# Optimization experiments

Measured on AMD Instinct MI355X. Metric: run time of the kernel, lower is better.

## Reference

```python
import jax, jax.numpy as jnp
import numpy as np

B, T, D, NH = 4, 2048, 1024, 16
HD = D // NH


def setup_inputs() -> dict:
    key = jax.random.key(0)
    ks = jax.random.split(key, 6)
    scale = 0.02
    x = jax.random.normal(ks[0], (B, T, D), dtype=jnp.float32)
    Wr = jax.random.normal(ks[1], (D, D), dtype=jnp.float32) * scale
    Wk = jax.random.normal(ks[2], (D, D), dtype=jnp.float32) * scale
    Wv = jax.random.normal(ks[3], (D, D), dtype=jnp.float32) * scale
    Ww = jax.random.normal(ks[4], (D, D), dtype=jnp.float32) * scale
    Wo = jax.random.normal(ks[5], (D, D), dtype=jnp.float32) * scale
    return {"x": x, "Wr": Wr, "Wk": Wk, "Wv": Wv, "Ww": Ww, "Wo": Wo}


def _rwkv7_forward(x, Wr, Wk, Wv, Ww, Wo):
    b, t, d = x.shape
    nh, hd = NH, d // NH
    # projections (F.linear: x @ W.T), no bias
    r = jax.nn.sigmoid(x @ Wr.T).reshape(b, t, nh, hd)
    k = (x @ Wk.T).reshape(b, t, nh, hd)
    v = (x @ Wv.T).reshape(b, t, nh, hd)
    w = (jax.nn.sigmoid(x @ Ww.T) * 0.99).reshape(b, t, nh, hd)

    def step(state, inp):
        # state: [B, nh, hd_v, hd_k]
        w_t, k_t, v_t, r_t = inp  # each [B, nh, hd]
        state = state * w_t[..., :, None] + v_t[..., :, None] * k_t[..., None, :]
        out_t = r_t * state.sum(-1)  # [B, nh, hd]
        return state, out_t

    seq = (jnp.moveaxis(w, 1, 0), jnp.moveaxis(k, 1, 0),
           jnp.moveaxis(v, 1, 0), jnp.moveaxis(r, 1, 0))  # time-major
    state0 = jnp.zeros((b, nh, hd, hd), dtype=x.dtype)
    _, outs = jax.lax.scan(step, state0, seq)  # [T, B, nh, hd]
    out = jnp.moveaxis(outs, 0, 1).reshape(b, t, d)

    # RMSNorm with eps=None -> torch uses dtype eps
    eps = jnp.asarray(jnp.finfo(out.dtype).eps, out.dtype)
    out = out * jax.lax.rsqrt(jnp.mean(out * out, axis=-1, keepdims=True) + eps)
    return out @ Wo.T


def reference(x, Wr, Wk, Wv, Ww, Wo):
    return _rwkv7_forward(x, Wr, Wk, Wv, Ww, Wo)
```

## Files before the change

### kernel.cpp

```cpp
#include <hip/hip_runtime.h>
#include <hip/hip_bf16.h>
#include <stdint.h>


#define BB 4
#define TT 2048
#define DD 1024
#define NHH 16
#define HDD 64
#define CC 64
#define LL 32
#define NCH 4096

using bf16 = __hip_bfloat16;
typedef __attribute__((ext_vector_type(8))) short bfrag8;
typedef __attribute__((ext_vector_type(4))) float f32x4;

__device__ __forceinline__ void async_ld16(const bf16* g, bf16* l) {
  __builtin_amdgcn_global_load_lds(
      (const __attribute__((address_space(1))) uint32_t*)g,
      (__attribute__((address_space(3))) uint32_t*)l, 16, 0, 0);
}

__device__ __forceinline__ float sigm(float x) {
  return __builtin_amdgcn_rcpf(1.0f + __expf(-x));
}
__device__ __forceinline__ float bf2f(bf16 h) {
  unsigned short u = *reinterpret_cast<unsigned short*>(&h);
  return __uint_as_float((unsigned)u << 16);
}
__device__ __forceinline__ unsigned short f2bfbits(float f) {
  bf16 b = __float2bfloat16(f);
  return *reinterpret_cast<unsigned short*>(&b);
}

__global__ __launch_bounds__(256)
void convert_kernel(const float* __restrict__ x,
                    const float* __restrict__ Wr, const float* __restrict__ Wv,
                    const float* __restrict__ Ww, const float* __restrict__ Wo,
                    const float* __restrict__ Wk,
                    bf16* __restrict__ x_c, bf16* __restrict__ W_c,
                    float* __restrict__ wks)
{
  if (blockIdx.x >= 12288) {
    const int gid = (blockIdx.x - 12288) * 256 + threadIdx.x;
    const int h = gid >> 10, c = gid & 1023;
    float s = 0.0f;
    for (int j = 0; j < 64; ++j)
      s += Wk[(long)((h << 6) + j) * 1024 + c];
    wks[gid] = s;
    return;
  }
  const long g = (long)blockIdx.x * 256 + threadIdx.x;
  const float* src; bf16* dst; long off4;
  if (g < 2097152) { src = x; dst = x_c; off4 = g; }
  else {
    long gg = g - 2097152;
    int wsel = (int)(gg >> 18);
    off4 = gg & 262143;
    src = (wsel == 0) ? Wr : (wsel == 1) ? Wv : (wsel == 2) ? Ww : Wo;
    dst = W_c + (long)wsel * 1048576;
  }
  float4 f = reinterpret_cast<const float4*>(src)[off4];
  ushort4 pk;
  pk.x = f2bfbits(f.x); pk.y = f2bfbits(f.y);
  pk.z = f2bfbits(f.z); pk.w = f2bfbits(f.w);
  reinterpret_cast<ushort4*>(dst)[off4] = pk;
}

__device__ __forceinline__ void gemm_mainloop(
    const bf16* __restrict__ A, const bf16* __restrict__ W,
    int blockM, int blockN, bf16* a_sh, bf16* b_sh, f32x4 acc[4][4])
{
  const int tid    = threadIdx.x;
  const int wave   = tid >> 6;
  const int lane   = tid & 63;
  const int lane15 = lane & 15;
  const int quad   = lane >> 4;
  const int waveM  = wave >> 1;
  const int waveN  = wave & 1;
  const int s_row  = (wave << 5) + (lane >> 3);
  const int s_col  = (((lane & 7) ^ ((lane >> 3) & 7)) << 3);

  const bf16* gA = A + ((long)(blockM * 128) + s_row) * 1024 + s_col;
  const bf16* gW = W + ((long)(blockN * 128) + s_row) * 1024 + s_col;
  bf16* la = a_sh + wave * 2048;
  bf16* lb = b_sh + wave * 2048;

  const int rsw = lane15 & 7;

  for (int k0 = 0; k0 < 1024; k0 += 64) {
#pragma unroll
    for (int it = 0; it < 4; ++it) {
      async_ld16(gA + k0 + it * 8 * 1024, la + it * 512);
      async_ld16(gW + k0 + it * 8 * 1024, lb + it * 512);
    }
    __syncthreads();
#pragma unroll
    for (int kh = 0; kh < 2; ++kh) {
      bfrag8 af[4], bfv[4];
      const int pc = ((kh * 4 + quad) ^ rsw) << 3;
#pragma unroll
      for (int mi = 0; mi < 4; ++mi)
        af[mi] = *reinterpret_cast<const bfrag8*>(a_sh + (waveM*64 + mi*16 + lane15)*64 + pc);
#pragma unroll
      for (int ni = 0; ni < 4; ++ni)
        bfv[ni] = *reinterpret_cast<const bfrag8*>(b_sh + (waveN*64 + ni*16 + lane15)*64 + pc);
#pragma unroll
      for (int mi = 0; mi < 4; ++mi)
#pragma unroll
        for (int ni = 0; ni < 4; ++ni)
          acc[mi][ni] = __builtin_amdgcn_mfma_f32_16x16x32_bf16(af[mi], bfv[ni], acc[mi][ni], 0, 0, 0);
    }
    __syncthreads();
  }
}

__global__ __launch_bounds__(256, 2)
void proj_kernel(const bf16* __restrict__ X, const bf16* __restrict__ W_c,
                 bf16* __restrict__ r_out, bf16* __restrict__ v_out,
                 bf16* __restrict__ w_out)
{
  __shared__ __align__(16) bf16 a_sh[128*64];
  __shared__ __align__(16) bf16 b_sh[128*64];
  const int f  = blockIdx.x;
  const int u  = f & 7;
  const int q  = f >> 3;
  const int n  = q & 7;
  const int p  = q >> 3;
  const int mh = p & 7;
  const int mode = p >> 3;
  const int m  = u + (mh << 3);

  const bf16* W = W_c + (long)mode * 1048576;
  f32x4 acc[4][4] = {};
  gemm_mainloop(X, W, m, n, a_sh, b_sh, acc);

  const int tid = threadIdx.x;
  const int wave = tid >> 6, lane = tid & 63;
  const int lane15 = lane & 15, quad = lane >> 4;
  const int waveM = wave >> 1, waveN = wave & 1;
  const int m_base = m * 128 + waveM * 64;
  const int n_base = n * 128 + waveN * 64;
  bf16* outp = (mode == 0) ? r_out : (mode == 1) ? v_out : w_out;
#pragma unroll
  for (int mi = 0; mi < 4; ++mi)
#pragma unroll
    for (int ni = 0; ni < 4; ++ni)
#pragma unroll
      for (int r = 0; r < 4; ++r) {
        float val = acc[mi][ni][r];
        if (mode == 0) val = sigm(val);
        else if (mode == 2) val = sigm(val) * 0.99f;
        int mm = m_base + mi*16 + quad*4 + r;
        int nn = n_base + ni*16 + lane15;
        outp[(long)mm * DD + nn] = __float2bfloat16(val);
      }
}

__global__ __launch_bounds__(256)
void ksum_kernel(const bf16* __restrict__ X, const float* __restrict__ wks,
                 float* __restrict__ ksum)
{
  __shared__ __align__(8) bf16 xs[DD];
  const int m = blockIdx.x;
  const int tid = threadIdx.x;
  *reinterpret_cast<ushort4*>(xs + tid*4) =
      *reinterpret_cast<const ushort4*>(X + (long)m * DD + tid*4);
  __syncthreads();
  const int wave = tid >> 6, lane = tid & 63;
  const int b = m >> 11, t = m & (TT - 1);
#pragma unroll
  for (int hi = 0; hi < 4; ++hi) {
    const int h = wave * 4 + hi;
    float acc = 0.0f;
#pragma unroll
    for (int i = 0; i < 16; ++i) {
      const int c = lane + (i << 6);
      acc += bf2f(xs[c]) * wks[h * DD + c];
    }
#pragma unroll
    for (int msk = 1; msk <= 32; msk <<= 1) acc += __shfl_xor(acc, msk);
    if (lane == 0) ksum[((long)(b * NHH + h)) * TT + t] = acc;
  }
}

__global__ __launch_bounds__(256)
void scanA_kernel(const bf16* __restrict__ v_buf, const bf16* __restrict__ w_buf,
                  const float* __restrict__ ksum,
                  float* __restrict__ Pbuf, float* __restrict__ Abuf)
{
  __shared__ float ks_sh[128];
  const int bh = blockIdx.x;
  const int b = bh >> 4, h = bh & 15;
  const int tid = threadIdx.x;
  const int i = tid & 63;
  const int cg = tid >> 6;
  const int chunk = blockIdx.y * 4 + cg;
  if (tid < 128) ks_sh[tid] = ksum[(long)bh * TT + blockIdx.y * 128 + tid];
  __syncthreads();
  const long base = (long)b * TT * DD + (long)(chunk * LL) * DD + h * HDD + i;
  float s = 0.0f, P = 1.0f;
#pragma unroll
  for (int j = 0; j < LL; ++j) {
    const long idx = base + (long)j * DD;
    float wv = bf2f(w_buf[idx]);
    float vv = bf2f(v_buf[idx]);
    s = fmaf(wv, s, vv * ks_sh[cg * LL + j]);
    P *= wv;
  }
  const int ch = bh * 64 + i;
  Pbuf[chunk * NCH + ch] = P;
  Abuf[chunk * NCH + ch] = s;
}

__global__ __launch_bounds__(256)
void scanB_kernel(const float* __restrict__ Pbuf, float* __restrict__ Abuf)
{
  const int ch = blockIdx.x * 256 + threadIdx.x;
  float carry = 0.0f;
  for (int c = 0; c < CC; ++c) {
    const int idx = c * NCH + ch;
    float p = Pbuf[idx];
    float a = Abuf[idx];
    Abuf[idx] = carry;
    carry = fmaf(p, carry, a);
  }
}

__global__ __launch_bounds__(256)
void scanC_kernel(const bf16* __restrict__ r_buf, bf16* v_so,
                  const bf16* __restrict__ w_buf, const float* __restrict__ ksum,
                  const float* __restrict__ Abuf)
{
  __shared__ float ks_sh[128];
  const int bh = blockIdx.x;
  const int b = bh >> 4, h = bh & 15;
  const int tid = threadIdx.x;
  const int i = tid & 63;
  const int cg = tid >> 6;
  const int chunk = blockIdx.y * 4 + cg;
  if (tid < 128) ks_sh[tid] = ksum[(long)bh * TT + blockIdx.y * 128 + tid];
  __syncthreads();
  const int ch = bh * 64 + i;
  const long base = (long)b * TT * DD + (long)(chunk * LL) * DD + h * HDD + i;
  float s = Abuf[chunk * NCH + ch];
#pragma unroll
  for (int j = 0; j < LL; ++j) {
    const long idx = base + (long)j * DD;
    float wv = bf2f(w_buf[idx]);
    float vv = bf2f(v_so[idx]);
    float rv = bf2f(r_buf[idx]);
    s = fmaf(wv, s, vv * ks_sh[cg * LL + j]);
    v_so[idx] = __float2bfloat16(rv * s);
  }
}

__global__ __launch_bounds__(256)
void rmsnorm_inplace(bf16* so)
{
  const long row = blockIdx.x;
  bf16* p = so + row * DD + threadIdx.x * 4;
  ushort4 u = *reinterpret_cast<const ushort4*>(p);
  float x0 = __uint_as_float((unsigned)u.x << 16);
  float x1 = __uint_as_float((unsigned)u.y << 16);
  float x2 = __uint_as_float((unsigned)u.z << 16);
  float x3 = __uint_as_float((unsigned)u.w << 16);
  float ss = x0*x0 + x1*x1 + x2*x2 + x3*x3;
#pragma unroll
  for (int m = 1; m <= 32; m <<= 1) ss += __shfl_xor(ss, m);
  __shared__ float part[4];
  if ((threadIdx.x & 63) == 0) part[threadIdx.x >> 6] = ss;
  __syncthreads();
  const float total = part[0] + part[1] + part[2] + part[3];
  const float scale = rsqrtf(total * (1.0f / DD) + 1.1920929e-07f);
  ushort4 pk;
  pk.x = f2bfbits(x0 * scale); pk.y = f2bfbits(x1 * scale);
  pk.z = f2bfbits(x2 * scale); pk.w = f2bfbits(x3 * scale);
  *reinterpret_cast<ushort4*>(p) = pk;
}

__global__ __launch_bounds__(256, 2)
void out_gemm_kernel(const bf16* __restrict__ A, const bf16* __restrict__ Wo_c,
                     float* __restrict__ out)
{
  __shared__ __align__(16) bf16 a_sh[128*64];
  __shared__ __align__(16) bf16 b_sh[128*64];
  const int f  = blockIdx.x;
  const int u  = f & 7;
  const int q  = f >> 3;
  const int n  = q & 7;
  const int mh = q >> 3;
  const int m  = u + (mh << 3);

  f32x4 acc[4][4] = {};
  gemm_mainloop(A, Wo_c, m, n, a_sh, b_sh, acc);

  const int tid = threadIdx.x;
  const int wave = tid >> 6, lane = tid & 63;
  const int lane15 = lane & 15, quad = lane >> 4;
  const int waveM = wave >> 1, waveN = wave & 1;
  const int m_base = m * 128 + waveM * 64;
  const int n_base = n * 128 + waveN * 64;
#pragma unroll
  for (int mi = 0; mi < 4; ++mi)
#pragma unroll
    for (int ni = 0; ni < 4; ++ni)
#pragma unroll
      for (int r = 0; r < 4; ++r) {
        int mm = m_base + mi*16 + quad*4 + r;
        int nn = n_base + ni*16 + lane15;
        out[(long)mm * DD + nn] = acc[mi][ni][r];
      }
}

extern "C" void kernel_launch(void* const* d_in, const int* in_sizes, int n_in,
                              void* d_out, int out_size, void* d_ws, size_t ws_size,
                              hipStream_t stream) {
  const float* x  = (const float*)d_in[0];
  const float* Wr = (const float*)d_in[1];
  const float* Wk = (const float*)d_in[2];
  const float* Wv = (const float*)d_in[3];
  const float* Ww = (const float*)d_in[4];
  const float* Wo = (const float*)d_in[5];

  const long NELT = (long)BB * TT * DD;
  bf16*  x_c  = (bf16*)d_ws;
  bf16*  W_c  = x_c + NELT;
  bf16*  v_so = W_c + 4 * 1048576;
  float* ksum = (float*)(v_so + NELT);
  float* wks  = ksum + (long)BB * NHH * TT;
  float* Pbuf = wks + NHH * DD;
  float* Abuf = Pbuf + (long)CC * NCH;

  bf16*  r_buf = (bf16*)d_out;
  bf16*  w_buf = (bf16*)d_out + NELT;
  float* out   = (float*)d_out;

  convert_kernel<<<dim3(12352), 256, 0, stream>>>(x, Wr, Wv, Ww, Wo, Wk, x_c, W_c, wks);
  proj_kernel<<<dim3(1536), 256, 0, stream>>>(x_c, W_c, r_buf, v_so, w_buf);
  ksum_kernel<<<dim3(BB * TT), 256, 0, stream>>>(x_c, wks, ksum);
  scanA_kernel<<<dim3(64, 16), 256, 0, stream>>>(v_so, w_buf, ksum, Pbuf, Abuf);
  scanB_kernel<<<dim3(16), 256, 0, stream>>>(Pbuf, Abuf);
  scanC_kernel<<<dim3(64, 16), 256, 0, stream>>>(r_buf, v_so, w_buf, ksum, Abuf);
  rmsnorm_inplace<<<dim3(BB * TT), 256, 0, stream>>>(v_so);
  out_gemm_kernel<<<dim3(512), 256, 0, stream>>>(v_so, W_c + 3 * 1048576, out);
}
```

Baseline: 236.5 us.

## Fuse RMSNorm into scan and GEMM epilogue; parallelize carry scan across waves

Removes the separate RMSNorm pass. scanC now accumulates per-row sums of squares with wave reductions and atomics, and the output GEMM applies the rsqrt scale in its epilogue, which is valid because the row scale commutes with the matmul. scanB is rewritten from a serial 64-step loop over 16 blocks into a wave-level Hillis-Steele scan using shuffles over 1024 blocks, and it also zeroes the sum-of-squares buffer, which reuses the x_c workspace. In exchange, scanC issues many atomics and the normalized values feed the GEMM unrounded, so rounding differs slightly from the old path.

```diff
diff --git a/kernel.cpp b/kernel.cpp
--- a/kernel.cpp
+++ b/kernel.cpp
@@ -215,23 +215,31 @@
 }
 
 __global__ __launch_bounds__(256)
-void scanB_kernel(const float* __restrict__ Pbuf, float* __restrict__ Abuf)
-{
-  const int ch = blockIdx.x * 256 + threadIdx.x;
-  float carry = 0.0f;
-  for (int c = 0; c < CC; ++c) {
-    const int idx = c * NCH + ch;
-    float p = Pbuf[idx];
-    float a = Abuf[idx];
-    Abuf[idx] = carry;
-    carry = fmaf(p, carry, a);
-  }
+void scanB_kernel(const float* __restrict__ Pbuf, float* __restrict__ Abuf,
+                  float* __restrict__ rowssq)
+{
+  const int tid  = threadIdx.x;
+  const int lane = tid & 63;
+  const int wch  = blockIdx.x * 4 + (tid >> 6);
+  const int idx  = lane * NCH + wch;
+  float p = Pbuf[idx];
+  float a = Abuf[idx];
+#pragma unroll
+  for (int d = 1; d < 64; d <<= 1) {
+    float al = __shfl_up(a, d);
+    float pl = __shfl_up(p, d);
+    if (lane >= d) { a = fmaf(p, al, a); p *= pl; }
+  }
+  float carry = __shfl_up(a, 1);
+  if (lane == 0) carry = 0.0f;
+  Abuf[idx] = carry;
+  if (blockIdx.x < 32) rowssq[blockIdx.x * 256 + tid] = 0.0f;
 }
 
 __global__ __launch_bounds__(256)
 void scanC_kernel(const bf16* __restrict__ r_buf, bf16* v_so,
                   const bf16* __restrict__ w_buf, const float* __restrict__ ksum,
-                  const float* __restrict__ Abuf)
+                  const float* __restrict__ Abuf, float* __restrict__ rowssq)
 {
   __shared__ float ks_sh[128];
   const int bh = blockIdx.x;
@@ -252,37 +260,19 @@
     float vv = bf2f(v_so[idx]);
     float rv = bf2f(r_buf[idx]);
     s = fmaf(wv, s, vv * ks_sh[cg * LL + j]);
-    v_so[idx] = __float2bfloat16(rv * s);
-  }
-}
-
-__global__ __launch_bounds__(256)
-void rmsnorm_inplace(bf16* so)
-{
-  const long row = blockIdx.x;
-  bf16* p = so + row * DD + threadIdx.x * 4;
-  ushort4 u = *reinterpret_cast<const ushort4*>(p);
-  float x0 = __uint_as_float((unsigned)u.x << 16);
-  float x1 = __uint_as_float((unsigned)u.y << 16);
-  float x2 = __uint_as_float((unsigned)u.z << 16);
-  float x3 = __uint_as_float((unsigned)u.w << 16);
-  float ss = x0*x0 + x1*x1 + x2*x2 + x3*x3;
-#pragma unroll
-  for (int m = 1; m <= 32; m <<= 1) ss += __shfl_xor(ss, m);
-  __shared__ float part[4];
-  if ((threadIdx.x & 63) == 0) part[threadIdx.x >> 6] = ss;
-  __syncthreads();
-  const float total = part[0] + part[1] + part[2] + part[3];
-  const float scale = rsqrtf(total * (1.0f / DD) + 1.1920929e-07f);
-  ushort4 pk;
-  pk.x = f2bfbits(x0 * scale); pk.y = f2bfbits(x1 * scale);
-  pk.z = f2bfbits(x2 * scale); pk.w = f2bfbits(x3 * scale);
-  *reinterpret_cast<ushort4*>(p) = pk;
+    unsigned short ob = f2bfbits(rv * s);
+    *reinterpret_cast<unsigned short*>(v_so + idx) = ob;
+    float vf = __uint_as_float((unsigned)ob << 16);
+    float ss = vf * vf;
+#pragma unroll
+    for (int msk = 1; msk <= 32; msk <<= 1) ss += __shfl_xor(ss, msk);
+    if (i == 0) atomicAdd(&rowssq[b * TT + chunk * LL + j], ss);
+  }
 }
 
 __global__ __launch_bounds__(256, 2)
 void out_gemm_kernel(const bf16* __restrict__ A, const bf16* __restrict__ Wo_c,
-                     float* __restrict__ out)
+                     const float* __restrict__ rowssq, float* __restrict__ out)
 {
   __shared__ __align__(16) bf16 a_sh[128*64];
   __shared__ __align__(16) bf16 b_sh[128*64];
@@ -305,13 +295,15 @@
 #pragma unroll
   for (int mi = 0; mi < 4; ++mi)
 #pragma unroll
-    for (int ni = 0; ni < 4; ++ni)
-#pragma unroll
-      for (int r = 0; r < 4; ++r) {
-        int mm = m_base + mi*16 + quad*4 + r;
+    for (int r = 0; r < 4; ++r) {
+      int mm = m_base + mi*16 + quad*4 + r;
+      float sc = rsqrtf(rowssq[mm] * (1.0f / DD) + 1.1920929e-07f);
+#pragma unroll
+      for (int ni = 0; ni < 4; ++ni) {
         int nn = n_base + ni*16 + lane15;
-        out[(long)mm * DD + nn] = acc[mi][ni][r];
+        out[(long)mm * DD + nn] = acc[mi][ni][r] * sc;
       }
+    }
 }
 
 extern "C" void kernel_launch(void* const* d_in, const int* in_sizes, int n_in,
@@ -332,6 +324,7 @@
   float* wks  = ksum + (long)BB * NHH * TT;
   float* Pbuf = wks + NHH * DD;
   float* Abuf = Pbuf + (long)CC * NCH;
+  float* rowssq = (float*)x_c;
 
   bf16*  r_buf = (bf16*)d_out;
   bf16*  w_buf = (bf16*)d_out + NELT;
@@ -341,8 +334,7 @@
   proj_kernel<<<dim3(1536), 256, 0, stream>>>(x_c, W_c, r_buf, v_so, w_buf);
   ksum_kernel<<<dim3(BB * TT), 256, 0, stream>>>(x_c, wks, ksum);
   scanA_kernel<<<dim3(64, 16), 256, 0, stream>>>(v_so, w_buf, ksum, Pbuf, Abuf);
-  scanB_kernel<<<dim3(16), 256, 0, stream>>>(Pbuf, Abuf);
-  scanC_kernel<<<dim3(64, 16), 256, 0, stream>>>(r_buf, v_so, w_buf, ksum, Abuf);
-  rmsnorm_inplace<<<dim3(BB * TT), 256, 0, stream>>>(v_so);
-  out_gemm_kernel<<<dim3(512), 256, 0, stream>>>(v_so, W_c + 3 * 1048576, out);
-}
+  scanB_kernel<<<dim3(1024), 256, 0, stream>>>(Pbuf, Abuf, rowssq);
+  scanC_kernel<<<dim3(64, 16), 256, 0, stream>>>(r_buf, v_so, w_buf, ksum, Abuf, rowssq);
+  out_gemm_kernel<<<dim3(512), 256, 0, stream>>>(v_so, W_c + 3 * 1048576, rowssq, out);
+}
```

After: 231.1 us. 2.3% less time.
